# Optimization experiments

Hardware: AMD Instinct MI355X
Metric: run time of the kernel (lower is better)

Reference implementation:

```python
import jax, jax.numpy as jnp
import numpy as np

WS = 4        # window_size
SS = 2        # shift_size
NH = 8        # num_heads
EPS = 1e-5    # LayerNorm eps (torch default)


def _rel_pos_index(ws):
    coords = np.stack(np.meshgrid(np.arange(ws), np.arange(ws), indexing='ij')).reshape(2, -1)
    rel = (coords[:, :, None] - coords[:, None, :]).transpose(1, 2, 0)
    rel[..., 0] += ws - 1
    rel[..., 1] += ws - 1
    rel[..., 0] *= 2 * ws - 1
    return rel.sum(-1)  # [N, N] ints

REL_IDX = _rel_pos_index(WS)


def _shift_mask(Hp, Wp, ws, ss):
    # standard Swin shifted-window region mask: 0 within region, -100 across regions
    img = np.zeros((Hp, Wp))
    cnt = 0
    for hs in (slice(0, -ws), slice(-ws, -ss), slice(-ss, None)):
        for wsl in (slice(0, -ws), slice(-ws, -ss), slice(-ss, None)):
            img[hs, wsl] = cnt
            cnt += 1
    mw = img.reshape(Hp // ws, ws, Wp // ws, ws).transpose(0, 2, 1, 3).reshape(-1, ws * ws)
    d = mw[:, None, :] - mw[:, :, None]
    return np.where(d != 0, -100.0, 0.0).astype(np.float32)  # [nW, N, N]


def _ln(x, g, b):
    m = jnp.mean(x, -1, keepdims=True)
    v = jnp.mean((x - m) ** 2, -1, keepdims=True)
    return (x - m) * jax.lax.rsqrt(v + EPS) * g + b


def setup_inputs() -> dict:
    key = jax.random.key(0)
    ks = jax.random.split(key, 8)
    D, F = 512, 1024
    rn = lambda k, s: (jax.random.normal(k, s, jnp.float32) * 0.02)
    return {
        'x': jax.random.normal(ks[0], (4, 64 * 128, D), jnp.float32),
        'g1': jnp.ones((D,), jnp.float32), 'beta1': jnp.zeros((D,), jnp.float32),
        'w_qkv': rn(ks[1], (3 * D, D)), 'b_qkv': jnp.zeros((3 * D,), jnp.float32),
        'rpb': rn(ks[2], ((2 * WS - 1) ** 2, NH)),
        'w_proj': rn(ks[3], (D, D)), 'b_proj': jnp.zeros((D,), jnp.float32),
        'g2': jnp.ones((D,), jnp.float32), 'beta2': jnp.zeros((D,), jnp.float32),
        'w1': rn(ks[4], (F, D)), 'b1': jnp.zeros((F,), jnp.float32),
        'w2': rn(ks[5], (D, F)), 'b2': jnp.zeros((D,), jnp.float32),
        'H': 64, 'W': 128,
    }


def reference(x, g1, beta1, w_qkv, b_qkv, rpb, w_proj, b_proj, g2, beta2, w1, b1, w2, b2, H, W):
    B, L, C = x.shape
    hd = C // NH
    scale = hd ** (-0.5)
    N = WS * WS
    Hp, Wp = H, W  # H, W chosen divisible by WS -> no padding branch
    nW = (Hp // WS) * (Wp // WS)

    shortcut = x
    h = _ln(x, g1, beta1).reshape(B, H, W, C)
    # cyclic shift
    h = jnp.roll(h, (-SS, -SS), axis=(1, 2))
    # window partition -> [B*nW, N, C]
    xw = h.reshape(B, Hp // WS, WS, Wp // WS, WS, C).transpose(0, 1, 3, 2, 4, 5).reshape(-1, N, C)

    qkv = (xw @ w_qkv.T + b_qkv).reshape(-1, N, 3, NH, hd).transpose(2, 0, 3, 1, 4)
    q, k, v = qkv[0] * scale, qkv[1], qkv[2]          # [B*nW, NH, N, hd]
    attn = jnp.einsum('whnd,whmd->whnm', q, k)        # [B*nW, NH, N, N]

    bias = rpb[REL_IDX.reshape(-1)].reshape(N, N, NH).transpose(2, 0, 1)  # [NH, N, N]
    attn = attn + bias[None]

    mask = jnp.asarray(_shift_mask(Hp, Wp, WS, SS))   # [nW, N, N]
    attn = attn.reshape(B, nW, NH, N, N) + mask[None, :, None]
    attn = jax.nn.softmax(attn.reshape(-1, NH, N, N), axis=-1)

    o = jnp.einsum('whnm,whmd->whnd', attn, v).transpose(0, 2, 1, 3).reshape(-1, N, C)
    o = o @ w_proj.T + b_proj
    # window reverse + reverse shift
    o = o.reshape(B, Hp // WS, Wp // WS, WS, WS, C).transpose(0, 1, 3, 2, 4, 5).reshape(B, Hp, Wp, C)
    o = jnp.roll(o, (SS, SS), axis=(1, 2)).reshape(B, H * W, C)

    x = shortcut + o
    h2 = _ln(x, g2, beta2)
    m = jax.nn.gelu(h2 @ w1.T + b1, approximate=False) @ w2.T + b2
    return x + m
```

## Files before the change

### kernel.cpp

```cpp
#include <hip/hip_runtime.h>
#include <hip/hip_bf16.h>
#include <math.h>

typedef __bf16 bf16_t;
typedef __bf16 bf16x8 __attribute__((ext_vector_type(8)));
typedef float f32x4 __attribute__((ext_vector_type(4)));


#define X1_OFF   0u
#define XW_OFF   67108864u
#define QKV_OFF  100663296u
#define WQ_OFF   201326592u
#define WP_OFF   202899456u
#define W1_OFF   203423744u
#define W2_OFF   204472320u
#define SV_OFF   205520896u
#define FLAG_OFF 205545472u

__device__ __forceinline__ int perm_row(int r) {
    int b   = r >> 13;
    int rem = r & 8191;
    int w   = rem >> 4;
    int n   = rem & 15;
    int wy  = w >> 5, wx = w & 31;
    int y   = wy * 4 + (n >> 2);
    int x   = wx * 4 + (n & 3);
    int ys  = (y + 2) & 63;
    int xs  = (x + 2) & 127;
    return (b << 13) + (ys << 7) + xs;
}

__device__ __forceinline__ void gld16(const void* g, void* l) {
    __builtin_amdgcn_global_load_lds(
        (const __attribute__((address_space(1))) unsigned int*)(unsigned long long)(uintptr_t)g,
        (__attribute__((address_space(3))) unsigned int*)(unsigned int)(uintptr_t)l,
        16, 0, 0);
}

__global__ __launch_bounds__(256) void k_probe(const unsigned short* __restrict__ x,
                                               int n, int* __restrict__ flag) {
    __shared__ int cnt;
    if (threadIdx.x == 0) cnt = 0;
    __syncthreads();
    int c = 0;
    for (int i = threadIdx.x; i < n; i += 256) {
        int e = (x[i] >> 7) & 0xFF;
        if (e >= 0xC0) c++;
    }
    atomicAdd(&cnt, c);
    __syncthreads();
    if (threadIdx.x == 0) *flag = (cnt > 8) ? 1 : 0;
}

__global__ __launch_bounds__(256) void k_cvt_bf16(const void* __restrict__ src,
                                                  bf16_t* __restrict__ dst, int n,
                                                  const int* __restrict__ flag) {
    int i = blockIdx.x * 256 + threadIdx.x;
    if (i >= n) return;
    dst[i] = (*flag) ? (bf16_t)((const float*)src)[i] : ((const bf16_t*)src)[i];
}

__global__ __launch_bounds__(256) void k_cvt_small(
        const void* g1, const void* be1, const void* bq, const void* bp,
        const void* g2, const void* be2, const void* b1, const void* b2,
        const void* rpb, float* __restrict__ dst, const int* __restrict__ flag) {
    int i = blockIdx.x * 256 + threadIdx.x;
    const void* src; int off;
    if      (i < 512)  { src = g1;  off = i; }
    else if (i < 1024) { src = be1; off = i - 512; }
    else if (i < 2560) { src = bq;  off = i - 1024; }
    else if (i < 3072) { src = bp;  off = i - 2560; }
    else if (i < 3584) { src = g2;  off = i - 3072; }
    else if (i < 4096) { src = be2; off = i - 3584; }
    else if (i < 5120) { src = b1;  off = i - 4096; }
    else if (i < 5632) { src = b2;  off = i - 5120; }
    else if (i < 6024) { src = rpb; off = i - 5632; }
    else return;
    dst[i] = (*flag) ? ((const float*)src)[off] : (float)((const bf16_t*)src)[off];
}

__global__ __launch_bounds__(256) void k_ln1(const void* __restrict__ x,
                                             const float* __restrict__ g,
                                             const float* __restrict__ be,
                                             bf16_t* __restrict__ xw,
                                             const int* __restrict__ flag) {
    int r    = blockIdx.x * 4 + (threadIdx.x >> 6);
    int lane = threadIdx.x & 63;
    int f    = *flag;
    long ro  = (long)perm_row(r) * 512;
    const float*  x32 = (const float*)x + ro;
    const bf16_t* x16 = (const bf16_t*)x + ro;
    int base = lane * 8;
    float v[8];
    float s = 0.f, ss = 0.f;
#pragma unroll
    for (int j = 0; j < 8; j++) {
        float t = f ? x32[base + j] : (float)x16[base + j];
        v[j] = t; s += t; ss += t * t;
    }
#pragma unroll
    for (int off = 32; off; off >>= 1) {
        s  += __shfl_down(s,  off, 64);
        ss += __shfl_down(ss, off, 64);
    }
    s  = __shfl(s, 0, 64);
    ss = __shfl(ss, 0, 64);
    float m   = s * (1.f / 512.f);
    float var = ss * (1.f / 512.f) - m * m;
    float inv = rsqrtf(var + 1e-5f);
    bf16_t* orow = xw + (long)r * 512;
#pragma unroll
    for (int j = 0; j < 8; j++)
        orow[base + j] = (bf16_t)((v[j] - m) * inv * g[base + j] + be[base + j]);
}

__global__ __launch_bounds__(256) void k_ln2(const float* __restrict__ x1,
                                             const float* __restrict__ g,
                                             const float* __restrict__ be,
                                             bf16_t* __restrict__ h2) {
    int r    = blockIdx.x * 4 + (threadIdx.x >> 6);
    int lane = threadIdx.x & 63;
    const float* xr = x1 + (long)r * 512;
    int base = lane * 8;
    float v[8];
    float s = 0.f, ss = 0.f;
#pragma unroll
    for (int j = 0; j < 8; j++) {
        float t = xr[base + j];
        v[j] = t; s += t; ss += t * t;
    }
#pragma unroll
    for (int off = 32; off; off >>= 1) {
        s  += __shfl_down(s,  off, 64);
        ss += __shfl_down(ss, off, 64);
    }
    s  = __shfl(s, 0, 64);
    ss = __shfl(ss, 0, 64);
    float m   = s * (1.f / 512.f);
    float var = ss * (1.f / 512.f) - m * m;
    float inv = rsqrtf(var + 1e-5f);
    bf16_t* orow = h2 + (long)r * 512;
#pragma unroll
    for (int j = 0; j < 8; j++)
        orow[base + j] = (bf16_t)((v[j] - m) * inv * g[base + j] + be[base + j]);
}

template<int EPI>
__global__ __launch_bounds__(512, 2) void k_gemm256(const bf16_t* __restrict__ A,
                                                    const bf16_t* __restrict__ Wt,
                                                    const float* __restrict__ bias,
                                                    void* __restrict__ out,
                                                    const void* __restrict__ res,
                                                    const int* __restrict__ flag,
                                                    int N, int K) {
    __shared__ __attribute__((aligned(16))) char smem[131072];
    int tid  = threadIdx.x;
    int lane = tid & 63, wv = tid >> 6;

    int nbx = N >> 8;
    int id  = blockIdx.x;
    int xb  = (id >> 3) % nbx;
    int yb  = ((id >> 3) / nbx) * 8 + (id & 7);
    int m0  = yb << 8, n0 = xb << 8;

    int srow = tid >> 2;
    int cg   = (tid & 3) ^ (srow & 3) ^ ((srow >> 2) & 3);
    const bf16_t* gA = A  + (long)(m0 + srow) * K + cg * 8;
    const bf16_t* gB = Wt + (long)(n0 + srow) * K + cg * 8;
    long rstep = (long)128 * K;
    int  l0 = wv * 1024, l1 = 8192 + wv * 1024;

    int S = K >> 5;

    gld16(gA,              smem + l0);
    gld16(gA + rstep,      smem + l1);
    gld16(gB,              smem + 16384 + l0);
    gld16(gB + rstep,      smem + 16384 + l1);
    gld16(gA + 32,         smem + 32768 + l0);
    gld16(gA + rstep + 32, smem + 32768 + l1);
    gld16(gB + 32,         smem + 32768 + 16384 + l0);
    gld16(gB + rstep + 32, smem + 32768 + 16384 + l1);

    int rr = lane & 15, quad = lane >> 4;
    int wh = wv >> 2, wq = wv & 3;
    int cA   = quad ^ (rr & 3) ^ ((rr >> 2) & 3);
    int aoff = (wh * 128 + rr) * 32 + cA * 8;
    int boff = 8192 + (wq * 64 + rr) * 32 + cA * 8;

    f32x4 acc[8][4];
#pragma unroll
    for (int mi = 0; mi < 8; mi++)
#pragma unroll
        for (int ni = 0; ni < 4; ni++) { f32x4 z = {0.f,0.f,0.f,0.f}; acc[mi][ni] = z; }

    for (int s = 0; s < S; ++s) {
        if (s + 2 < S) {
            char* db = smem + ((s + 2) & 3) * 32768;
            long  ko = (long)(s + 2) * 32;
            gld16(gA + ko,          db + l0);
            gld16(gA + rstep + ko,  db + l1);
            gld16(gB + ko,          db + 16384 + l0);
            gld16(gB + rstep + ko,  db + 16384 + l1);
            asm volatile("s_waitcnt vmcnt(8)" ::: "memory");
        } else if (s + 2 == S) {
            asm volatile("s_waitcnt vmcnt(4)" ::: "memory");
        } else {
            asm volatile("s_waitcnt vmcnt(0)" ::: "memory");
        }
        __builtin_amdgcn_sched_barrier(0);
        __builtin_amdgcn_s_barrier();
        __builtin_amdgcn_sched_barrier(0);

        const bf16_t* sb = (const bf16_t*)(smem + (s & 3) * 32768);
        const bf16_t* pa = sb + aoff;
        const bf16_t* pb = sb + boff;
        bf16x8 bg[4], af[4];
#pragma unroll
        for (int ni = 0; ni < 4; ni++) bg[ni] = *(const bf16x8*)(pb + ni * 512);
#pragma unroll
        for (int mi = 0; mi < 4; mi++) af[mi] = *(const bf16x8*)(pa + mi * 512);
        __builtin_amdgcn_s_setprio(1);
#pragma unroll
        for (int mi = 0; mi < 4; mi++)
#pragma unroll
            for (int ni = 0; ni < 4; ni++)
                acc[mi][ni] = __builtin_amdgcn_mfma_f32_16x16x32_bf16(af[mi], bg[ni], acc[mi][ni], 0, 0, 0);
        __builtin_amdgcn_s_setprio(0);
#pragma unroll
        for (int mi = 0; mi < 4; mi++) af[mi] = *(const bf16x8*)(pa + (mi + 4) * 512);
        __builtin_amdgcn_s_setprio(1);
#pragma unroll
        for (int mi = 0; mi < 4; mi++)
#pragma unroll
            for (int ni = 0; ni < 4; ni++)
                acc[mi + 4][ni] = __builtin_amdgcn_mfma_f32_16x16x32_bf16(af[mi], bg[ni], acc[mi + 4][ni], 0, 0, 0);
        __builtin_amdgcn_s_setprio(0);
    }

    __builtin_amdgcn_sched_barrier(0);
    __builtin_amdgcn_s_barrier();
    __builtin_amdgcn_sched_barrier(0);

    float* sc  = (float*)smem + wv * 4096;
    int f      = (EPI == 1 || EPI == 3) ? *flag : 0;
    int rl     = lane >> 3;
    int cl8    = (lane & 7) * 8;
    int colw   = n0 + wq * 64 + cl8;
    f32x4 b0   = *(const f32x4*)(bias + colw);
    f32x4 b1   = *(const f32x4*)(bias + colw + 4);

#pragma unroll
    for (int h = 0; h < 2; ++h) {
#pragma unroll
        for (int mi2 = 0; mi2 < 4; ++mi2)
#pragma unroll
            for (int ni = 0; ni < 4; ++ni) {
                int ch = ni * 4 + (rr >> 2);
#pragma unroll
                for (int i = 0; i < 4; ++i) {
                    int r = mi2 * 16 + quad * 4 + i;
                    sc[r * 64 + (((ch ^ (r & 15)) << 2) | (rr & 3))] = acc[h * 4 + mi2][ni][i];
                }
            }
#pragma unroll
        for (int p = 0; p < 8; ++p) {
            int r   = p * 8 + rl;
            int sw  = r & 15;
            int ch0 = (lane & 7) * 2;
            f32x4 v0 = *(const f32x4*)(sc + r * 64 + (((ch0    ) ^ sw) << 2));
            f32x4 v1 = *(const f32x4*)(sc + r * 64 + (((ch0 + 1) ^ sw) << 2));
            int row = m0 + wh * 128 + h * 64 + r;
            v0 += b0; v1 += b1;

            if (EPI == 0) {
                bf16x8 ob;
#pragma unroll
                for (int c = 0; c < 4; c++) { ob[c] = (bf16_t)v0[c]; ob[c + 4] = (bf16_t)v1[c]; }
                *(bf16x8*)((bf16_t*)out + (long)row * N + colw) = ob;
            } else if (EPI == 1) {
                long o = (long)perm_row(row) * 512 + colw;
                if (f) {
                    f32x4 r0 = *(const f32x4*)((const float*)res + o);
                    f32x4 r1 = *(const f32x4*)((const float*)res + o + 4);
                    v0 += r0; v1 += r1;
                } else {
                    bf16x8 rb = *(const bf16x8*)((const bf16_t*)res + o);
#pragma unroll
                    for (int c = 0; c < 4; c++) { v0[c] += (float)rb[c]; v1[c] += (float)rb[c + 4]; }
                }
                *(f32x4*)((float*)out + o)     = v0;
                *(f32x4*)((float*)out + o + 4) = v1;
            } else if (EPI == 2) {
                bf16x8 ob;
#pragma unroll
                for (int c = 0; c < 4; c++) {
                    float a0 = v0[c], a1 = v1[c];
                    ob[c]     = (bf16_t)(0.5f * a0 * (1.f + erff(a0 * 0.70710678118654752f)));
                    ob[c + 4] = (bf16_t)(0.5f * a1 * (1.f + erff(a1 * 0.70710678118654752f)));
                }
                *(bf16x8*)((bf16_t*)out + (long)row * N + colw) = ob;
            } else {
                long o = (long)row * 512 + colw;
                f32x4 r0 = *(const f32x4*)((const float*)res + o);
                f32x4 r1 = *(const f32x4*)((const float*)res + o + 4);
                v0 += r0; v1 += r1;
                if (f) {
                    *(f32x4*)((float*)out + o)     = v0;
                    *(f32x4*)((float*)out + o + 4) = v1;
                } else {
                    bf16x8 ob;
#pragma unroll
                    for (int c = 0; c < 4; c++) { ob[c] = (bf16_t)v0[c]; ob[c + 4] = (bf16_t)v1[c]; }
                    *(bf16x8*)((bf16_t*)out + o) = ob;
                }
            }
        }
    }
}

__global__ __launch_bounds__(256) void k_attn(const bf16_t* __restrict__ qkv,
                                              const float* __restrict__ rpb,
                                              bf16_t* __restrict__ O) {
    __shared__ float q[16][68], k[16][68], v[16][68];
    __shared__ float S[16][17];

    int blk = blockIdx.x;
    int h   = blk & 7;
    int w   = blk >> 3;
    int tid = threadIdx.x;

    int n0 = tid >> 4;
    int d0 = (tid & 15) * 4;
    const bf16_t* base = qkv + (long)(w * 16 + n0) * 1536 + h * 64 + d0;
#pragma unroll
    for (int j = 0; j < 4; j++) {
        q[n0][d0 + j] = (float)base[j] * 0.125f;
        k[n0][d0 + j] = (float)base[512 + j];
        v[n0][d0 + j] = (float)base[1024 + j];
    }
    __syncthreads();

    int i = tid >> 4, j = tid & 15;
    float s = 0.f;
#pragma unroll
    for (int d = 0; d < 64; d++) s += q[i][d] * k[j][d];

    int iy = i >> 2, ix = i & 3, jy = j >> 2, jx = j & 3;
    s += rpb[((iy - jy + 3) * 7 + (ix - jx + 3)) * 8 + h];

    int wl = w & 511;
    int wy = wl >> 5, wx = wl & 31;
    int yi = wy * 4 + iy, xi = wx * 4 + ix;
    int yj = wy * 4 + jy, xj = wx * 4 + jx;
    int ri = (yi < 60 ? 0 : (yi < 62 ? 1 : 2)) * 3 + (xi < 124 ? 0 : (xi < 126 ? 1 : 2));
    int rj = (yj < 60 ? 0 : (yj < 62 ? 1 : 2)) * 3 + (xj < 124 ? 0 : (xj < 126 ? 1 : 2));
    if (ri != rj) s -= 100.f;
    S[i][j] = s;
    __syncthreads();

    if (tid < 16) {
        float mx = -1e30f;
#pragma unroll
        for (int c = 0; c < 16; c++) mx = fmaxf(mx, S[tid][c]);
        float sum = 0.f;
#pragma unroll
        for (int c = 0; c < 16; c++) { float e = expf(S[tid][c] - mx); S[tid][c] = e; sum += e; }
        float invs = 1.f / sum;
#pragma unroll
        for (int c = 0; c < 16; c++) S[tid][c] *= invs;
    }
    __syncthreads();

#pragma unroll
    for (int t = 0; t < 4; t++) {
        int e  = tid + t * 256;
        int oi = e >> 6, od = e & 63;
        float acc = 0.f;
#pragma unroll
        for (int c = 0; c < 16; c++) acc += S[oi][c] * v[c][od];
        O[(long)(w * 16 + oi) * 512 + h * 64 + od] = (bf16_t)acc;
    }
}

extern "C" void kernel_launch(void* const* d_in, const int* in_sizes, int n_in,
                              void* d_out, int out_size, void* d_ws, size_t ws_size,
                              hipStream_t stream) {
    char* ws = (char*)d_ws;
    float*  x1   = (float*)(ws + X1_OFF);
    bf16_t* xw   = (bf16_t*)(ws + XW_OFF);
    bf16_t* qkv  = (bf16_t*)(ws + QKV_OFF);
    bf16_t* wq_b = (bf16_t*)(ws + WQ_OFF);
    bf16_t* wp_b = (bf16_t*)(ws + WP_OFF);
    bf16_t* w1_b = (bf16_t*)(ws + W1_OFF);
    bf16_t* w2_b = (bf16_t*)(ws + W2_OFF);
    float*  sv   = (float*)(ws + SV_OFF);
    int*    flag = (int*)(ws + FLAG_OFF);

    k_probe<<<1, 256, 0, stream>>>((const unsigned short*)d_in[0], 4096, flag);
    k_cvt_bf16<<<3072, 256, 0, stream>>>(d_in[3],  wq_b, 786432, flag);
    k_cvt_bf16<<<1024, 256, 0, stream>>>(d_in[6],  wp_b, 262144, flag);
    k_cvt_bf16<<<2048, 256, 0, stream>>>(d_in[10], w1_b, 524288, flag);
    k_cvt_bf16<<<2048, 256, 0, stream>>>(d_in[12], w2_b, 524288, flag);
    k_cvt_small<<<24,  256, 0, stream>>>(d_in[1], d_in[2], d_in[4], d_in[7],
                                         d_in[8], d_in[9], d_in[11], d_in[13],
                                         d_in[5], sv, flag);

    k_ln1<<<dim3(8192), dim3(256), 0, stream>>>(d_in[0], sv, sv + 512, xw, flag);
    k_gemm256<0><<<dim3(768), dim3(512), 0, stream>>>(xw, wq_b, sv + 1024, qkv, nullptr, flag, 1536, 512);
    k_attn<<<dim3(16384), dim3(256), 0, stream>>>(qkv, sv + 5632, xw );
    k_gemm256<1><<<dim3(256), dim3(512), 0, stream>>>(xw, wp_b, sv + 2560, x1, d_in[0], flag, 512, 512);
    k_ln2<<<dim3(8192), dim3(256), 0, stream>>>(x1, sv + 3072, sv + 3584, xw );
    k_gemm256<2><<<dim3(512), dim3(512), 0, stream>>>(xw, w1_b, sv + 4096, qkv , nullptr, flag, 1024, 512);
    k_gemm256<3><<<dim3(256), dim3(512), 0, stream>>>(qkv, w2_b, sv + 5120, d_out, x1, flag, 512, 1024);
}
```

Before: 522.7 us.

## Restructure GEMM main loop to BK=64 double-buffer with four-phase quadrant pipelining

The 256x256 GEMM kernel moves from a four-slot ring of BK=32 stages to two BK=64 buffers. Each K-step is split into four phases over A/B half-tiles, and the global-to-LDS copy of the next stage is interleaved between phases. The LDS swizzle changes to an 8-chunk XOR layout, the warp-to-tile mapping is altered, and the epilogue is rewritten to match. The aim is better overlap of loads with MFMA and fewer barriers per unit of K, at the cost of more barriers per step and more complex wait-count bookkeeping.

```diff
diff --git a/kernel.cpp b/kernel.cpp
--- a/kernel.cpp
+++ b/kernel.cpp
@@ -36,6 +36,9 @@
         (__attribute__((address_space(3))) unsigned int*)(unsigned int)(uintptr_t)l,
         16, 0, 0);
 }
+
+#define SBAR __builtin_amdgcn_sched_barrier(0)
+#define BARRIER do { SBAR; __builtin_amdgcn_s_barrier(); SBAR; } while (0)
 
 __global__ __launch_bounds__(256) void k_probe(const unsigned short* __restrict__ x,
                                                int n, int* __restrict__ flag) {
@@ -163,29 +166,18 @@
     int yb  = ((id >> 3) / nbx) * 8 + (id & 7);
     int m0  = yb << 8, n0 = xb << 8;
 
-    int srow = tid >> 2;
-    int cg   = (tid & 3) ^ (srow & 3) ^ ((srow >> 2) & 3);
+    int srow = tid >> 3;
+    int cg   = (tid & 7) ^ (srow & 7);
     const bf16_t* gA = A  + (long)(m0 + srow) * K + cg * 8;
     const bf16_t* gB = Wt + (long)(n0 + srow) * K + cg * 8;
-    long rstep = (long)128 * K;
-    int  l0 = wv * 1024, l1 = 8192 + wv * 1024;
-
-    int S = K >> 5;
-
-    gld16(gA,              smem + l0);
-    gld16(gA + rstep,      smem + l1);
-    gld16(gB,              smem + 16384 + l0);
-    gld16(gB + rstep,      smem + 16384 + l1);
-    gld16(gA + 32,         smem + 32768 + l0);
-    gld16(gA + rstep + 32, smem + 32768 + l1);
-    gld16(gB + 32,         smem + 32768 + 16384 + l0);
-    gld16(gB + rstep + 32, smem + 32768 + 16384 + l1);
+    long r64 = (long)64 * K;
 
     int rr = lane & 15, quad = lane >> 4;
     int wh = wv >> 2, wq = wv & 3;
-    int cA   = quad ^ (rr & 3) ^ ((rr >> 2) & 3);
-    int aoff = (wh * 128 + rr) * 32 + cA * 8;
-    int boff = 8192 + (wq * 64 + rr) * 32 + cA * 8;
+    int lA  = (wh * 64 + rr) * 128;
+    int lB  = (wq * 32 + rr) * 128;
+    int ck0 = (quad ^ (rr & 7)) * 16;
+    int ck1 = ck0 ^ 64;
 
     f32x4 acc[8][4];
 #pragma unroll
@@ -193,92 +185,127 @@
 #pragma unroll
         for (int ni = 0; ni < 4; ni++) { f32x4 z = {0.f,0.f,0.f,0.f}; acc[mi][ni] = z; }
 
-    for (int s = 0; s < S; ++s) {
-        if (s + 2 < S) {
-            char* db = smem + ((s + 2) & 3) * 32768;
-            long  ko = (long)(s + 2) * 32;
-            gld16(gA + ko,          db + l0);
-            gld16(gA + rstep + ko,  db + l1);
-            gld16(gB + ko,          db + 16384 + l0);
-            gld16(gB + rstep + ko,  db + 16384 + l1);
-            asm volatile("s_waitcnt vmcnt(8)" ::: "memory");
-        } else if (s + 2 == S) {
-            asm volatile("s_waitcnt vmcnt(4)" ::: "memory");
-        } else {
-            asm volatile("s_waitcnt vmcnt(0)" ::: "memory");
-        }
-        __builtin_amdgcn_sched_barrier(0);
-        __builtin_amdgcn_s_barrier();
-        __builtin_amdgcn_sched_barrier(0);
-
-        const bf16_t* sb = (const bf16_t*)(smem + (s & 3) * 32768);
-        const bf16_t* pa = sb + aoff;
-        const bf16_t* pb = sb + boff;
-        bf16x8 bg[4], af[4];
-#pragma unroll
-        for (int ni = 0; ni < 4; ni++) bg[ni] = *(const bf16x8*)(pb + ni * 512);
-#pragma unroll
-        for (int mi = 0; mi < 4; mi++) af[mi] = *(const bf16x8*)(pa + mi * 512);
-        __builtin_amdgcn_s_setprio(1);
-#pragma unroll
-        for (int mi = 0; mi < 4; mi++)
-#pragma unroll
-            for (int ni = 0; ni < 4; ni++)
-                acc[mi][ni] = __builtin_amdgcn_mfma_f32_16x16x32_bf16(af[mi], bg[ni], acc[mi][ni], 0, 0, 0);
-        __builtin_amdgcn_s_setprio(0);
-#pragma unroll
-        for (int mi = 0; mi < 4; mi++) af[mi] = *(const bf16x8*)(pa + (mi + 4) * 512);
-        __builtin_amdgcn_s_setprio(1);
-#pragma unroll
-        for (int mi = 0; mi < 4; mi++)
-#pragma unroll
-            for (int ni = 0; ni < 4; ni++)
-                acc[mi + 4][ni] = __builtin_amdgcn_mfma_f32_16x16x32_bf16(af[mi], bg[ni], acc[mi + 4][ni], 0, 0, 0);
-        __builtin_amdgcn_s_setprio(0);
-    }
-
-    __builtin_amdgcn_sched_barrier(0);
-    __builtin_amdgcn_s_barrier();
-    __builtin_amdgcn_sched_barrier(0);
-
-    float* sc  = (float*)smem + wv * 4096;
-    int f      = (EPI == 1 || EPI == 3) ? *flag : 0;
-    int rl     = lane >> 3;
-    int cl8    = (lane & 7) * 8;
-    int colw   = n0 + wq * 64 + cl8;
-    f32x4 b0   = *(const f32x4*)(bias + colw);
-    f32x4 b1   = *(const f32x4*)(bias + colw + 4);
-
-#pragma unroll
-    for (int h = 0; h < 2; ++h) {
-#pragma unroll
-        for (int mi2 = 0; mi2 < 4; ++mi2)
-#pragma unroll
-            for (int ni = 0; ni < 4; ++ni) {
-                int ch = ni * 4 + (rr >> 2);
-#pragma unroll
-                for (int i = 0; i < 4; ++i) {
-                    int r = mi2 * 16 + quad * 4 + i;
-                    sc[r * 64 + (((ch ^ (r & 15)) << 2) | (rr & 3))] = acc[h * 4 + mi2][ni][i];
-                }
-            }
+    int S = K >> 6;
+
+    gld16(gA,             smem + 0     + wv * 1024);
+    gld16(gA + r64,       smem + 8192  + wv * 1024);
+    gld16(gB,             smem + 32768 + wv * 1024);
+    gld16(gB + r64,       smem + 40960 + wv * 1024);
+    gld16(gB + 2 * r64,   smem + 49152 + wv * 1024);
+    gld16(gB + 3 * r64,   smem + 57344 + wv * 1024);
+    gld16(gA + 2 * r64,   smem + 16384 + wv * 1024);
+    gld16(gA + 3 * r64,   smem + 24576 + wv * 1024);
+
+    bf16x8 af[4][2], bg[2][2];
+
+#define DO_PHASE(AH, BH, LOADA)                                               \
+    do {                                                                      \
+        if (LOADA) {                                                          \
+            _Pragma("unroll") for (int mi = 0; mi < 4; mi++) {                \
+                af[mi][0] = *(const bf16x8*)(bc + (AH)*16384 + lA + mi*2048 + ck0); \
+                af[mi][1] = *(const bf16x8*)(bc + (AH)*16384 + lA + mi*2048 + ck1); \
+            }                                                                 \
+        }                                                                     \
+        _Pragma("unroll") for (int ni = 0; ni < 2; ni++) {                    \
+            bg[ni][0] = *(const bf16x8*)(bc + 32768 + (BH)*16384 + lB + ni*2048 + ck0); \
+            bg[ni][1] = *(const bf16x8*)(bc + 32768 + (BH)*16384 + lB + ni*2048 + ck1); \
+        }                                                                     \
+        asm volatile("s_waitcnt lgkmcnt(0)" ::: "memory"); SBAR;              \
+        __builtin_amdgcn_s_setprio(1);                                        \
+        _Pragma("unroll") for (int mi = 0; mi < 4; mi++)                      \
+            _Pragma("unroll") for (int ni = 0; ni < 2; ni++)                  \
+                _Pragma("unroll") for (int kk = 0; kk < 2; kk++)              \
+                    acc[(AH)*4 + mi][(BH)*2 + ni] =                           \
+                        __builtin_amdgcn_mfma_f32_16x16x32_bf16(              \
+                            af[mi][kk], bg[ni][kk], acc[(AH)*4 + mi][(BH)*2 + ni], 0, 0, 0); \
+        __builtin_amdgcn_s_setprio(0);                                        \
+    } while (0)
+
+#define STAGE(GP, SLOT)                                                       \
+    do { gld16((GP) + kn,       bn + (SLOT) + wv * 1024);                     \
+         gld16((GP) + r64 + kn, bn + (SLOT) + 8192 + wv * 1024); } while (0)
+
+    for (int t = 0; t < S - 1; ++t) {
+        char* bc = smem + (t & 1) * 65536;
+        char* bn = smem + ((t & 1) ^ 1) * 65536;
+        long  kn = (long)(t + 1) * 64;
+        STAGE(gA, 0);
+        asm volatile("s_waitcnt vmcnt(6)" ::: "memory");
+        BARRIER;
+        DO_PHASE(0, 0, 1);
+        BARRIER;
+        STAGE(gB, 32768);
+        asm volatile("s_waitcnt vmcnt(6)" ::: "memory");
+        BARRIER;
+        DO_PHASE(0, 1, 0);
+        BARRIER;
+        STAGE(gB + 2 * r64, 49152);
+        asm volatile("s_waitcnt vmcnt(6)" ::: "memory");
+        BARRIER;
+        DO_PHASE(1, 0, 1);
+        BARRIER;
+        STAGE(gA + 2 * r64, 16384);
+        DO_PHASE(1, 1, 0);
+        BARRIER;
+    }
+    {
+        char* bc = smem + ((S - 1) & 1) * 65536;
+        asm volatile("s_waitcnt vmcnt(4)" ::: "memory");
+        BARRIER;
+        DO_PHASE(0, 0, 1);
+        BARRIER;
+        asm volatile("s_waitcnt vmcnt(2)" ::: "memory");
+        BARRIER;
+        DO_PHASE(0, 1, 0);
+        BARRIER;
+        asm volatile("s_waitcnt vmcnt(0)" ::: "memory");
+        BARRIER;
+        DO_PHASE(1, 0, 1);
+        BARRIER;
+        DO_PHASE(1, 1, 0);
+        BARRIER;
+    }
+#undef DO_PHASE
+#undef STAGE
+
+    float* sc = (float*)(smem + wv * 16384);
+    int f    = (EPI == 1 || EPI == 3) ? *flag : 0;
+    int j8   = lane & 7;
+    int rl   = lane >> 3;
+    int colg = n0 + wq * 32 + (j8 >> 2) * 128 + ((j8 * 8) & 31);
+    f32x4 b0 = *(const f32x4*)(bias + colg);
+    f32x4 b1 = *(const f32x4*)(bias + colg + 4);
+
+#pragma unroll
+    for (int ah = 0; ah < 2; ++ah) {
+#pragma unroll
+        for (int bh = 0; bh < 2; ++bh)
+#pragma unroll
+            for (int ni = 0; ni < 2; ++ni)
+#pragma unroll
+                for (int mi = 0; mi < 4; ++mi)
+#pragma unroll
+                    for (int i = 0; i < 4; ++i) {
+                        int r  = mi * 16 + quad * 4 + i;
+                        int cl = bh * 32 + ni * 16 + rr;
+                        sc[r * 64 + ((((cl >> 2) ^ (r & 15)) << 2) | (cl & 3))] =
+                            acc[ah * 4 + mi][bh * 2 + ni][i];
+                    }
 #pragma unroll
         for (int p = 0; p < 8; ++p) {
-            int r   = p * 8 + rl;
-            int sw  = r & 15;
-            int ch0 = (lane & 7) * 2;
-            f32x4 v0 = *(const f32x4*)(sc + r * 64 + (((ch0    ) ^ sw) << 2));
-            f32x4 v1 = *(const f32x4*)(sc + r * 64 + (((ch0 + 1) ^ sw) << 2));
-            int row = m0 + wh * 128 + h * 64 + r;
+            int r = p * 8 + rl;
+            f32x4 v0 = *(const f32x4*)(sc + r * 64 + (((2 * j8)     ^ (r & 15)) << 2));
+            f32x4 v1 = *(const f32x4*)(sc + r * 64 + (((2 * j8 + 1) ^ (r & 15)) << 2));
+            int row = m0 + ah * 128 + wh * 64 + r;
             v0 += b0; v1 += b1;
 
             if (EPI == 0) {
                 bf16x8 ob;
 #pragma unroll
                 for (int c = 0; c < 4; c++) { ob[c] = (bf16_t)v0[c]; ob[c + 4] = (bf16_t)v1[c]; }
-                *(bf16x8*)((bf16_t*)out + (long)row * N + colw) = ob;
+                *(bf16x8*)((bf16_t*)out + (long)row * N + colg) = ob;
             } else if (EPI == 1) {
-                long o = (long)perm_row(row) * 512 + colw;
+                long o = (long)perm_row(row) * 512 + colg;
                 if (f) {
                     f32x4 r0 = *(const f32x4*)((const float*)res + o);
                     f32x4 r1 = *(const f32x4*)((const float*)res + o + 4);
@@ -298,9 +325,9 @@
                     ob[c]     = (bf16_t)(0.5f * a0 * (1.f + erff(a0 * 0.70710678118654752f)));
                     ob[c + 4] = (bf16_t)(0.5f * a1 * (1.f + erff(a1 * 0.70710678118654752f)));
                 }
-                *(bf16x8*)((bf16_t*)out + (long)row * N + colw) = ob;
+                *(bf16x8*)((bf16_t*)out + (long)row * N + colg) = ob;
             } else {
-                long o = (long)row * 512 + colw;
+                long o = (long)row * 512 + colg;
                 f32x4 r0 = *(const f32x4*)((const float*)res + o);
                 f32x4 r1 = *(const f32x4*)((const float*)res + o + 4);
                 v0 += r0; v1 += r1;
```

After: 442.0 us. 15.4% less time.
